# Performance work log

Measured on AMD Instinct MI355X. Metric: run time of the kernel, lower is better.

The kernel has to match this reference:

```python
import jax, jax.numpy as jnp
import numpy as np

B, TQ, TK = 4, 256, 256
Q, K, H = 256, 256, 256


def setup_inputs() -> dict:
    key = jax.random.key(0)
    ks = jax.random.split(key, 10)
    s = 0.05
    return {
        "queries": jax.random.normal(ks[0], (B, TQ, Q), dtype=jnp.float32),
        "keys": jax.random.normal(ks[1], (B, TK, K), dtype=jnp.float32),
        # lengths in [T//2, T] so no fully-masked query rows (torch would NaN there too)
        "query_lengths": jax.random.randint(ks[2], (B,), TQ // 2, TQ + 1),
        "key_lengths": jax.random.randint(ks[3], (B,), TK // 2, TK + 1),
        # nn.Linear(Q+K, H): weight applied as x @ W1; torch concat order is [keys, queries]
        "W1": jax.random.normal(ks[4], (K + Q, H), dtype=jnp.float32) * s,
        "b1": jax.random.normal(ks[5], (H,), dtype=jnp.float32) * s,
        "W2": jax.random.normal(ks[6], (H, H), dtype=jnp.float32) * s,
        "b2": jax.random.normal(ks[7], (H,), dtype=jnp.float32) * s,
        "W3": jax.random.normal(ks[8], (H, 1), dtype=jnp.float32) * s,
        "b3": jax.random.normal(ks[9], (1,), dtype=jnp.float32) * s,
    }


def reference(queries, keys, query_lengths, key_lengths, W1, b1, W2, b2, W3, b3):
    Bn, Tq, Qd = queries.shape
    Tk, Kd = keys.shape[1], keys.shape[2]
    # Split the first linear: concat([keys, queries]) @ W1 == keys@W1[:K] + queries@W1[K:]
    kh = jnp.einsum("bkd,dh->bkh", keys, W1[:Kd])      # [B,Tk,H]
    qh = jnp.einsum("bqd,dh->bqh", queries, W1[Kd:])   # [B,Tq,H]
    h = jax.nn.relu(qh[:, :, None, :] + kh[:, None, :, :] + b1)  # [B,Tq,Tk,H]
    h = jax.nn.relu(jnp.einsum("bqkh,hg->bqkg", h, W2) + b2)     # [B,Tq,Tk,H]
    scores = jnp.einsum("bqkh,h->bqk", h, W3[:, 0]) + b3[0]       # [B,Tq,Tk]
    # mask True where position is padding (query OR key out of range)
    mask = (jnp.arange(Tq)[None, :, None] >= query_lengths[:, None, None]) | (
        jnp.arange(Tk)[None, None, :] >= key_lengths[:, None, None]
    )
    scores = jnp.where(mask, -1e30, scores)
    probs = jax.nn.softmax(scores, axis=-1)
    probs = jnp.where(mask, 0.0, probs)
    return jnp.einsum("bqk,bkd->bqd", probs, keys)  # [B,Tq,K]
```

## Files before the change

### kernel.cpp

```cpp
#include <hip/hip_runtime.h>
#include <cstdint>

#define BATCH 4
#define TQ 256
#define TK 256
#define DIM 256
#define HD 256

typedef _Float16 f16x8 __attribute__((ext_vector_type(8)));
typedef float f32x4 __attribute__((ext_vector_type(4)));

union U4H8 { uint4 u; f16x8 v; };

#define KEEP(x) asm volatile("" : "+v"(x))

__device__ __forceinline__ unsigned short f2h(float f) {
    _Float16 h = (_Float16)f;
    unsigned short u;
    __builtin_memcpy(&u, &h, 2);
    return u;
}

__device__ __forceinline__ uint32_t pk2h(float a, float b) {
    auto r = __builtin_amdgcn_cvt_pkrtz(a, b);
    uint32_t w;
    __builtin_memcpy(&w, &r, 4);
    return w;
}

__global__ __launch_bounds__(256) void prep_all(
    const float* __restrict__ queries, const float* __restrict__ keys,
    const float* __restrict__ W1, const float* __restrict__ b1,
    const float* __restrict__ W2,
    float* __restrict__ qh, float* __restrict__ kh,
    unsigned short* __restrict__ W2T) {
    int i = blockIdx.x;
    int t = threadIdx.x;
    if (i >= 512) {
        __shared__ float tile[32][33];
        int bi = i - 512;
        int tx = t & 31, ty = t >> 5;
        int tc = (bi & 7) * 32, tn = (bi >> 3) * 32;
#pragma unroll
        for (int r = 0; r < 4; ++r)
            tile[ty + r * 8][tx] = W2[(tc + ty + r * 8) * HD + tn + tx];
        __syncthreads();
#pragma unroll
        for (int r = 0; r < 4; ++r)
            W2T[(tn + ty + r * 8) * HD + tc + tx] = f2h(tile[tx][ty + r * 8]);
        return;
    }
    bool isQ = i < 256;
    int r0 = (i & 255) * 4;
    const float* X = isQ ? queries : keys;
    const float* W = W1 + (isQ ? DIM * HD : 0);
    float* O = isQ ? qh : kh;
    __shared__ float xs[4][DIM];
#pragma unroll
    for (int r = 0; r < 4; ++r) xs[r][t] = X[(r0 + r) * DIM + t];
    __syncthreads();
    float acc[4] = {0.f, 0.f, 0.f, 0.f};
#pragma unroll 8
    for (int d = 0; d < DIM; ++d) {
        float w = W[d * HD + t];
#pragma unroll
        for (int r = 0; r < 4; ++r) acc[r] = fmaf(xs[r][d], w, acc[r]);
    }
    float bias = isQ ? b1[t] : 0.f;
#pragma unroll
    for (int r = 0; r < 4; ++r) O[(r0 + r) * HD + t] = acc[r] + bias;
}

__global__ __launch_bounds__(256, 2) void mlp_attn(
    const float* __restrict__ qh, const float* __restrict__ kh,
    const unsigned short* __restrict__ W2T,
    const float* __restrict__ b2, const float* __restrict__ W3,
    const float* __restrict__ keys,
    const int* __restrict__ qlens, const int* __restrict__ klens,
    float* __restrict__ out) {
    int orig = blockIdx.x;
    int bid = ((orig & 7) << 6) | (orig >> 3);
    int b = bid >> 7;
    int q0 = (bid & 127) << 1;
    int t = threadIdx.x;
    int qlen = qlens[b];
    float* orow = out + (b * TQ + q0) * DIM;
    if (q0 >= qlen) { orow[t] = 0.f; orow[DIM + t] = 0.f; return; }
    bool v1 = (q0 + 1) < qlen;
    int klen = klens[b];
    int nch = (klen + 31) >> 5;

    __shared__ uint4 Afrag[2][8][4][64];
    __shared__ float sprt[4][2][TK];
    __shared__ float srow[2][TK];
    __shared__ float Qlds[2][HD];
    __shared__ float red[16];

    int w = t >> 6, lane = t & 63;
    int col = lane & 15, quad = lane >> 4;

    int nb = w << 6;
    uint4 bfr[4][8];
#pragma unroll
    for (int nt = 0; nt < 4; ++nt) {
        int n = nb + (nt << 4) + col;
        const uint4* r = (const uint4*)(W2T + n * HD) + quad;
#pragma unroll
        for (int s = 0; s < 8; ++s) bfr[nt][s] = r[s * 4];
    }
    float b2v[4][4], w3v[4][4];
#pragma unroll
    for (int nt = 0; nt < 4; ++nt)
#pragma unroll
        for (int r = 0; r < 4; ++r) {
            int n = nb + (nt << 4) + (quad << 2) + r;
            b2v[nt][r] = b2[n];
            w3v[nt][r] = W3[n];
        }

    int qsel = w >> 1;
    int rsub = ((w & 1) << 4) | col;
    const float* kbase = kh + (b * TK + rsub) * HD + (quad << 3);

    {
        const float* qrowg = qh + (b * TQ + q0 + qsel) * HD + (quad << 3);
        const float* krow = kbase;
        uint4* as = &Afrag[0][0][w][lane];
#pragma unroll
        for (int s = 0; s < 8; ++s) {
            const float4 k0 = *(const float4*)(krow + s * 32);
            const float4 k1 = *(const float4*)(krow + s * 32 + 4);
            const float4 qa = *(const float4*)(qrowg + s * 32);
            const float4 qb = *(const float4*)(qrowg + s * 32 + 4);
            uint4 wv;
            wv.x = pk2h(fmaxf(k0.x + qa.x, 0.f), fmaxf(k0.y + qa.y, 0.f));
            wv.y = pk2h(fmaxf(k0.z + qa.z, 0.f), fmaxf(k0.w + qa.w, 0.f));
            wv.z = pk2h(fmaxf(k1.x + qb.x, 0.f), fmaxf(k1.y + qb.y, 0.f));
            wv.w = pk2h(fmaxf(k1.z + qb.z, 0.f), fmaxf(k1.w + qb.w, 0.f));
            as[s * 256] = wv;
        }
    }
    Qlds[0][t] = qh[(b * TQ + q0) * HD + t];
    Qlds[1][t] = qh[(b * TQ + q0 + 1) * HD + t];

#pragma unroll
    for (int nt = 0; nt < 4; ++nt)
#pragma unroll
        for (int s = 0; s < 8; ++s) {
            KEEP(bfr[nt][s].x); KEEP(bfr[nt][s].y);
            KEEP(bfr[nt][s].z); KEEP(bfr[nt][s].w);
        }

    __syncthreads();

    auto sloop = [&](int cur, int mt, f32x4* acc) {
#pragma unroll
        for (int s = 0; s < 8; ++s) {
            U4H8 au;
            au.u = Afrag[cur][s][mt][lane];
#pragma unroll
            for (int nt = 0; nt < 4; ++nt) {
                U4H8 bu;
                bu.u = bfr[nt][s];
                acc[nt] = __builtin_amdgcn_mfma_f32_16x16x32_f16(
                    bu.v, au.v, acc[nt], 0, 0, 0);
            }
        }
    };
    auto epi = [&](int c, int mt, const f32x4* acc) {
        int hf = mt >> 1, m2 = mt & 1;
        float part = 0.f;
#pragma unroll
        for (int nt = 0; nt < 4; ++nt)
#pragma unroll
            for (int r = 0; r < 4; ++r)
                part = fmaf(fmaxf(acc[nt][r] + b2v[nt][r], 0.f), w3v[nt][r], part);
        part += __shfl_xor(part, 16, 64);
        part += __shfl_xor(part, 32, 64);
        if (quad == 0)
            sprt[w][hf][(c << 5) | (m2 << 4) | col] = part;
    };

    for (int c = 0; c < nch; ++c) {
        int cur = c & 1;
        bool stg = (c + 1 < nch);
        const float* krow = kbase + (((c + 1) << 5)) * HD;
        uint4* as1 = &Afrag[cur ^ 1][0][w][lane];

        auto wslot = [&](int s, const float4& k0, const float4& k1) {
            const float4 qa = *(const float4*)&Qlds[qsel][s * 32 + (quad << 3)];
            const float4 qb = *(const float4*)&Qlds[qsel][s * 32 + (quad << 3) + 4];
            uint4 wv;
            wv.x = pk2h(fmaxf(k0.x + qa.x, 0.f), fmaxf(k0.y + qa.y, 0.f));
            wv.y = pk2h(fmaxf(k0.z + qa.z, 0.f), fmaxf(k0.w + qa.w, 0.f));
            wv.z = pk2h(fmaxf(k1.x + qb.x, 0.f), fmaxf(k1.y + qb.y, 0.f));
            wv.w = pk2h(fmaxf(k1.z + qb.z, 0.f), fmaxf(k1.w + qb.w, 0.f));
            as1[s * 256] = wv;
        };

        float4 A0, A1, A2, A3, B0, B1, B2, B3;
        if (stg) {
            A0 = *(const float4*)(krow);       A1 = *(const float4*)(krow + 4);
            A2 = *(const float4*)(krow + 32);  A3 = *(const float4*)(krow + 36);
        }
        __builtin_amdgcn_sched_barrier(0);

        {
            f32x4 acc[4] = {};
            sloop(cur, 0, acc);
            if (stg) {
                wslot(0, A0, A1); wslot(1, A2, A3);
                B0 = *(const float4*)(krow + 64);  B1 = *(const float4*)(krow + 68);
                B2 = *(const float4*)(krow + 96);  B3 = *(const float4*)(krow + 100);
            }
            __builtin_amdgcn_sched_barrier(0);
            epi(c, 0, acc);
            if (stg) {
                wslot(2, B0, B1); wslot(3, B2, B3);
                A0 = *(const float4*)(krow + 128); A1 = *(const float4*)(krow + 132);
                A2 = *(const float4*)(krow + 160); A3 = *(const float4*)(krow + 164);
            }
            __builtin_amdgcn_sched_barrier(0);
        }
        {
            f32x4 acc[4] = {};
            sloop(cur, 1, acc);
            if (stg) {
                wslot(4, A0, A1); wslot(5, A2, A3);
                B0 = *(const float4*)(krow + 192); B1 = *(const float4*)(krow + 196);
                B2 = *(const float4*)(krow + 224); B3 = *(const float4*)(krow + 228);
            }
            __builtin_amdgcn_sched_barrier(0);
            epi(c, 1, acc);
            if (stg) { wslot(6, B0, B1); wslot(7, B2, B3); }
        }
        {
            f32x4 acc[4] = {};
            sloop(cur, 2, acc);
            epi(c, 2, acc);
        }
        {
            f32x4 acc[4] = {};
            sloop(cur, 3, acc);
            epi(c, 3, acc);
        }
        __syncthreads();
    }

    float s0 = -3.4e38f, s1 = -3.4e38f;
    if (t < klen) {
        s0 = (sprt[0][0][t] + sprt[1][0][t]) + (sprt[2][0][t] + sprt[3][0][t]);
        s1 = (sprt[0][1][t] + sprt[1][1][t]) + (sprt[2][1][t] + sprt[3][1][t]);
    }
    float m0 = s0, m1 = s1;
#pragma unroll
    for (int off = 1; off < 64; off <<= 1) {
        m0 = fmaxf(m0, __shfl_xor(m0, off, 64));
        m1 = fmaxf(m1, __shfl_xor(m1, off, 64));
    }
    if (lane == 0) { red[w] = m0; red[8 + w] = m1; }
    __syncthreads();
    m0 = fmaxf(fmaxf(red[0], red[1]), fmaxf(red[2], red[3]));
    m1 = fmaxf(fmaxf(red[8], red[9]), fmaxf(red[10], red[11]));
    float e0 = (t < klen) ? __expf(s0 - m0) : 0.f;
    float e1 = (t < klen) ? __expf(s1 - m1) : 0.f;
    float u0 = e0, u1 = e1;
#pragma unroll
    for (int off = 1; off < 64; off <<= 1) {
        u0 += __shfl_xor(u0, off, 64);
        u1 += __shfl_xor(u1, off, 64);
    }
    if (lane == 0) { red[4 + w] = u0; red[12 + w] = u1; }
    __syncthreads();
    float d0 = red[4] + red[5] + red[6] + red[7];
    float d1 = red[12] + red[13] + red[14] + red[15];
    srow[0][t] = e0 / d0;
    srow[1][t] = e1 / d1;
    __syncthreads();

    float a0 = 0.f, a1 = 0.f;
    const float* kp = keys + b * TK * DIM + t;
#pragma unroll 8
    for (int k = 0; k < klen; ++k) {
        float v = kp[k * DIM];
        a0 = fmaf(srow[0][k], v, a0);
        a1 = fmaf(srow[1][k], v, a1);
    }
    orow[t] = a0;
    orow[DIM + t] = v1 ? a1 : 0.f;
}

extern "C" void kernel_launch(void* const* d_in, const int* in_sizes, int n_in,
                              void* d_out, int out_size, void* d_ws, size_t ws_size,
                              hipStream_t stream) {
    (void)in_sizes; (void)n_in; (void)out_size; (void)ws_size;
    const float* queries = (const float*)d_in[0];
    const float* keys    = (const float*)d_in[1];
    const int*   qlens   = (const int*)d_in[2];
    const int*   klens   = (const int*)d_in[3];
    const float* W1      = (const float*)d_in[4];
    const float* b1      = (const float*)d_in[5];
    const float* W2      = (const float*)d_in[6];
    const float* b2      = (const float*)d_in[7];
    const float* W3      = (const float*)d_in[8];
    float* out = (float*)d_out;

    float* qh = (float*)d_ws;
    float* kh = qh + BATCH * TQ * HD;
    unsigned short* W2T = (unsigned short*)(kh + BATCH * TK * HD);

    prep_all<<<576, 256, 0, stream>>>(queries, keys, W1, b1, W2, qh, kh, W2T);
    mlp_attn<<<BATCH * TQ / 2, 256, 0, stream>>>(
        qh, kh, W2T, b2, W3, keys, qlens, klens, out);
}
```

Baseline: 129.8 us.

## Use atomic work-queue persistent blocks with smaller 16-key chunks

The attention kernel now pulls (batch, query-pair) tasks from a global atomic counter that prep_all resets, instead of a fixed block-to-task mapping. Inactive query pairs finish quickly and free the block for other work. The key chunk size drops from 32 to 16 rows, and each wave builds half the A-fragment slices. This is meant to balance load across batches whose valid lengths differ and to cut the shared memory per block. The cost is two extra barriers plus an atomic per task, and twice as many chunk iterations, each with its own barrier.

```diff
diff --git a/kernel.cpp b/kernel.cpp
--- a/kernel.cpp
+++ b/kernel.cpp
@@ -6,6 +6,7 @@
 #define TK 256
 #define DIM 256
 #define HD 256
+#define NTASK 512
 
 typedef _Float16 f16x8 __attribute__((ext_vector_type(8)));
 typedef float f32x4 __attribute__((ext_vector_type(4)));
@@ -33,10 +34,11 @@
     const float* __restrict__ W1, const float* __restrict__ b1,
     const float* __restrict__ W2,
     float* __restrict__ qh, float* __restrict__ kh,
-    unsigned short* __restrict__ W2T) {
+    unsigned short* __restrict__ W2T, int* __restrict__ cnt) {
     int i = blockIdx.x;
     int t = threadIdx.x;
     if (i >= 512) {
+        if (i == 512 && t == 0) *cnt = 0;
         __shared__ float tile[32][33];
         int bi = i - 512;
         int tx = t & 31, ty = t >> 5;
@@ -77,38 +79,28 @@
     const float* __restrict__ b2, const float* __restrict__ W3,
     const float* __restrict__ keys,
     const int* __restrict__ qlens, const int* __restrict__ klens,
-    float* __restrict__ out) {
-    int orig = blockIdx.x;
-    int bid = ((orig & 7) << 6) | (orig >> 3);
-    int b = bid >> 7;
-    int q0 = (bid & 127) << 1;
+    float* __restrict__ out, int* __restrict__ gcnt) {
     int t = threadIdx.x;
-    int qlen = qlens[b];
-    float* orow = out + (b * TQ + q0) * DIM;
-    if (q0 >= qlen) { orow[t] = 0.f; orow[DIM + t] = 0.f; return; }
-    bool v1 = (q0 + 1) < qlen;
-    int klen = klens[b];
-    int nch = (klen + 31) >> 5;
-
-    __shared__ uint4 Afrag[2][8][4][64];
+    int w = t >> 6, lane = t & 63;
+    int col = lane & 15, quad = lane >> 4;
+
+    __shared__ uint4 Afrag[2][8][2][64];
     __shared__ float sprt[4][2][TK];
     __shared__ float srow[2][TK];
     __shared__ float Qlds[2][HD];
     __shared__ float red[16];
-
-    int w = t >> 6, lane = t & 63;
-    int col = lane & 15, quad = lane >> 4;
+    __shared__ int tsk;
 
     int nb = w << 6;
-    uint4 bfr[4][8];
+    uint4 afr[4][8];
+    float b2v[4][4], w3v[4][4];
 #pragma unroll
     for (int nt = 0; nt < 4; ++nt) {
         int n = nb + (nt << 4) + col;
         const uint4* r = (const uint4*)(W2T + n * HD) + quad;
 #pragma unroll
-        for (int s = 0; s < 8; ++s) bfr[nt][s] = r[s * 4];
+        for (int s = 0; s < 8; ++s) afr[nt][s] = r[s * 4];
     }
-    float b2v[4][4], w3v[4][4];
 #pragma unroll
     for (int nt = 0; nt < 4; ++nt)
 #pragma unroll
@@ -117,58 +109,32 @@
             b2v[nt][r] = b2[n];
             w3v[nt][r] = W3[n];
         }
-
-    int qsel = w >> 1;
-    int rsub = ((w & 1) << 4) | col;
-    const float* kbase = kh + (b * TK + rsub) * HD + (quad << 3);
-
-    {
-        const float* qrowg = qh + (b * TQ + q0 + qsel) * HD + (quad << 3);
-        const float* krow = kbase;
-        uint4* as = &Afrag[0][0][w][lane];
+#pragma unroll
+    for (int nt = 0; nt < 4; ++nt)
 #pragma unroll
         for (int s = 0; s < 8; ++s) {
-            const float4 k0 = *(const float4*)(krow + s * 32);
-            const float4 k1 = *(const float4*)(krow + s * 32 + 4);
-            const float4 qa = *(const float4*)(qrowg + s * 32);
-            const float4 qb = *(const float4*)(qrowg + s * 32 + 4);
-            uint4 wv;
-            wv.x = pk2h(fmaxf(k0.x + qa.x, 0.f), fmaxf(k0.y + qa.y, 0.f));
-            wv.y = pk2h(fmaxf(k0.z + qa.z, 0.f), fmaxf(k0.w + qa.w, 0.f));
-            wv.z = pk2h(fmaxf(k1.x + qb.x, 0.f), fmaxf(k1.y + qb.y, 0.f));
-            wv.w = pk2h(fmaxf(k1.z + qb.z, 0.f), fmaxf(k1.w + qb.w, 0.f));
-            as[s * 256] = wv;
-        }
-    }
-    Qlds[0][t] = qh[(b * TQ + q0) * HD + t];
-    Qlds[1][t] = qh[(b * TQ + q0 + 1) * HD + t];
-
-#pragma unroll
-    for (int nt = 0; nt < 4; ++nt)
-#pragma unroll
-        for (int s = 0; s < 8; ++s) {
-            KEEP(bfr[nt][s].x); KEEP(bfr[nt][s].y);
-            KEEP(bfr[nt][s].z); KEEP(bfr[nt][s].w);
-        }
-
-    __syncthreads();
-
-    auto sloop = [&](int cur, int mt, f32x4* acc) {
+            KEEP(afr[nt][s].x); KEEP(afr[nt][s].y);
+            KEEP(afr[nt][s].z); KEEP(afr[nt][s].w);
+        }
+
+    int mt = w >> 1;
+    int sb = (w & 1) << 2;
+
+    auto sloop = [&](int cur, int p, f32x4* acc) {
 #pragma unroll
         for (int s = 0; s < 8; ++s) {
             U4H8 au;
-            au.u = Afrag[cur][s][mt][lane];
+            au.u = Afrag[cur][s][p][lane];
 #pragma unroll
             for (int nt = 0; nt < 4; ++nt) {
                 U4H8 bu;
-                bu.u = bfr[nt][s];
+                bu.u = afr[nt][s];
                 acc[nt] = __builtin_amdgcn_mfma_f32_16x16x32_f16(
                     bu.v, au.v, acc[nt], 0, 0, 0);
             }
         }
     };
-    auto epi = [&](int c, int mt, const f32x4* acc) {
-        int hf = mt >> 1, m2 = mt & 1;
+    auto epi = [&](int c, int p, const f32x4* acc) {
         float part = 0.f;
 #pragma unroll
         for (int nt = 0; nt < 4; ++nt)
@@ -178,116 +144,139 @@
         part += __shfl_xor(part, 16, 64);
         part += __shfl_xor(part, 32, 64);
         if (quad == 0)
-            sprt[w][hf][(c << 5) | (m2 << 4) | col] = part;
+            sprt[w][p][(c << 4) | col] = part;
     };
 
-    for (int c = 0; c < nch; ++c) {
-        int cur = c & 1;
-        bool stg = (c + 1 < nch);
-        const float* krow = kbase + (((c + 1) << 5)) * HD;
-        uint4* as1 = &Afrag[cur ^ 1][0][w][lane];
-
-        auto wslot = [&](int s, const float4& k0, const float4& k1) {
-            const float4 qa = *(const float4*)&Qlds[qsel][s * 32 + (quad << 3)];
-            const float4 qb = *(const float4*)&Qlds[qsel][s * 32 + (quad << 3) + 4];
-            uint4 wv;
-            wv.x = pk2h(fmaxf(k0.x + qa.x, 0.f), fmaxf(k0.y + qa.y, 0.f));
-            wv.y = pk2h(fmaxf(k0.z + qa.z, 0.f), fmaxf(k0.w + qa.w, 0.f));
-            wv.z = pk2h(fmaxf(k1.x + qb.x, 0.f), fmaxf(k1.y + qb.y, 0.f));
-            wv.w = pk2h(fmaxf(k1.z + qb.z, 0.f), fmaxf(k1.w + qb.w, 0.f));
-            as1[s * 256] = wv;
-        };
-
-        float4 A0, A1, A2, A3, B0, B1, B2, B3;
-        if (stg) {
-            A0 = *(const float4*)(krow);       A1 = *(const float4*)(krow + 4);
-            A2 = *(const float4*)(krow + 32);  A3 = *(const float4*)(krow + 36);
-        }
-        __builtin_amdgcn_sched_barrier(0);
+    for (;;) {
+        if (t == 0) tsk = atomicAdd(gcnt, 1);
+        __syncthreads();
+        int task = tsk;
+        __syncthreads();
+        if (task >= NTASK) break;
+        int b = task >> 7;
+        int q0 = (task & 127) << 1;
+        int qlen = qlens[b];
+        float* orow = out + ((size_t)b * TQ + q0) * DIM;
+        if (q0 >= qlen) { orow[t] = 0.f; orow[DIM + t] = 0.f; continue; }
+        bool v1 = (q0 + 1) < qlen;
+        int klen = klens[b];
+        int nch = (klen + 15) >> 4;
+
+        const float* kb_t = kh + ((size_t)b * TK + col) * HD + (quad << 3);
 
         {
-            f32x4 acc[4] = {};
-            sloop(cur, 0, acc);
+            const float* qg = qh + ((size_t)b * TQ + q0 + mt) * HD + (quad << 3);
+            uint4* as = &Afrag[0][0][mt][lane];
+#pragma unroll
+            for (int j = 0; j < 4; ++j) {
+                int s = sb + j;
+                const float4 k0 = *(const float4*)(kb_t + s * 32);
+                const float4 k1 = *(const float4*)(kb_t + s * 32 + 4);
+                const float4 qa = *(const float4*)(qg + s * 32);
+                const float4 qb = *(const float4*)(qg + s * 32 + 4);
+                uint4 wv;
+                wv.x = pk2h(fmaxf(k0.x + qa.x, 0.f), fmaxf(k0.y + qa.y, 0.f));
+                wv.y = pk2h(fmaxf(k0.z + qa.z, 0.f), fmaxf(k0.w + qa.w, 0.f));
+                wv.z = pk2h(fmaxf(k1.x + qb.x, 0.f), fmaxf(k1.y + qb.y, 0.f));
+                wv.w = pk2h(fmaxf(k1.z + qb.z, 0.f), fmaxf(k1.w + qb.w, 0.f));
+                as[s * 128] = wv;
+            }
+        }
+        Qlds[0][t] = qh[((size_t)b * TQ + q0) * HD + t];
+        Qlds[1][t] = qh[((size_t)b * TQ + q0 + 1) * HD + t];
+        __syncthreads();
+
+        for (int c = 0; c < nch; ++c) {
+            int cur = c & 1;
+            bool stg = (c + 1 < nch);
+            const float* kr = kb_t + (((c + 1) << 4)) * HD;
+            uint4* as1 = &Afrag[cur ^ 1][0][mt][lane];
+
+            auto wslot = [&](int s, const float4& k0, const float4& k1) {
+                const float4 qa = *(const float4*)&Qlds[mt][s * 32 + (quad << 3)];
+                const float4 qb = *(const float4*)&Qlds[mt][s * 32 + (quad << 3) + 4];
+                uint4 wv;
+                wv.x = pk2h(fmaxf(k0.x + qa.x, 0.f), fmaxf(k0.y + qa.y, 0.f));
+                wv.y = pk2h(fmaxf(k0.z + qa.z, 0.f), fmaxf(k0.w + qa.w, 0.f));
+                wv.z = pk2h(fmaxf(k1.x + qb.x, 0.f), fmaxf(k1.y + qb.y, 0.f));
+                wv.w = pk2h(fmaxf(k1.z + qb.z, 0.f), fmaxf(k1.w + qb.w, 0.f));
+                as1[s * 128] = wv;
+            };
+
+            float4 A0, A1, A2, A3, B0, B1, B2, B3;
             if (stg) {
-                wslot(0, A0, A1); wslot(1, A2, A3);
-                B0 = *(const float4*)(krow + 64);  B1 = *(const float4*)(krow + 68);
-                B2 = *(const float4*)(krow + 96);  B3 = *(const float4*)(krow + 100);
+                A0 = *(const float4*)(kr + sb * 32);
+                A1 = *(const float4*)(kr + sb * 32 + 4);
+                A2 = *(const float4*)(kr + (sb + 1) * 32);
+                A3 = *(const float4*)(kr + (sb + 1) * 32 + 4);
             }
             __builtin_amdgcn_sched_barrier(0);
-            epi(c, 0, acc);
-            if (stg) {
-                wslot(2, B0, B1); wslot(3, B2, B3);
-                A0 = *(const float4*)(krow + 128); A1 = *(const float4*)(krow + 132);
-                A2 = *(const float4*)(krow + 160); A3 = *(const float4*)(krow + 164);
-            }
-            __builtin_amdgcn_sched_barrier(0);
-        }
-        {
-            f32x4 acc[4] = {};
-            sloop(cur, 1, acc);
-            if (stg) {
-                wslot(4, A0, A1); wslot(5, A2, A3);
-                B0 = *(const float4*)(krow + 192); B1 = *(const float4*)(krow + 196);
-                B2 = *(const float4*)(krow + 224); B3 = *(const float4*)(krow + 228);
-            }
-            __builtin_amdgcn_sched_barrier(0);
-            epi(c, 1, acc);
-            if (stg) { wslot(6, B0, B1); wslot(7, B2, B3); }
-        }
-        {
-            f32x4 acc[4] = {};
-            sloop(cur, 2, acc);
-            epi(c, 2, acc);
-        }
-        {
-            f32x4 acc[4] = {};
-            sloop(cur, 3, acc);
-            epi(c, 3, acc);
-        }
-        __syncthreads();
+
+            {
+                f32x4 acc[4] = {};
+                sloop(cur, 0, acc);
+                if (stg) {
+                    wslot(sb, A0, A1); wslot(sb + 1, A2, A3);
+                    B0 = *(const float4*)(kr + (sb + 2) * 32);
+                    B1 = *(const float4*)(kr + (sb + 2) * 32 + 4);
+                    B2 = *(const float4*)(kr + (sb + 3) * 32);
+                    B3 = *(const float4*)(kr + (sb + 3) * 32 + 4);
+                }
+                __builtin_amdgcn_sched_barrier(0);
+                epi(c, 0, acc);
+            }
+            {
+                f32x4 acc[4] = {};
+                sloop(cur, 1, acc);
+                if (stg) { wslot(sb + 2, B0, B1); wslot(sb + 3, B2, B3); }
+                __builtin_amdgcn_sched_barrier(0);
+                epi(c, 1, acc);
+            }
+            __syncthreads();
+        }
+
+        float s0 = -3.4e38f, s1 = -3.4e38f;
+        if (t < klen) {
+            s0 = (sprt[0][0][t] + sprt[1][0][t]) + (sprt[2][0][t] + sprt[3][0][t]);
+            s1 = (sprt[0][1][t] + sprt[1][1][t]) + (sprt[2][1][t] + sprt[3][1][t]);
+        }
+        float m0 = s0, m1 = s1;
+#pragma unroll
+        for (int off = 1; off < 64; off <<= 1) {
+            m0 = fmaxf(m0, __shfl_xor(m0, off, 64));
+            m1 = fmaxf(m1, __shfl_xor(m1, off, 64));
+        }
+        if (lane == 0) { red[w] = m0; red[8 + w] = m1; }
+        __syncthreads();
+        m0 = fmaxf(fmaxf(red[0], red[1]), fmaxf(red[2], red[3]));
+        m1 = fmaxf(fmaxf(red[8], red[9]), fmaxf(red[10], red[11]));
+        float e0 = (t < klen) ? __expf(s0 - m0) : 0.f;
+        float e1 = (t < klen) ? __expf(s1 - m1) : 0.f;
+        float u0 = e0, u1 = e1;
+#pragma unroll
+        for (int off = 1; off < 64; off <<= 1) {
+            u0 += __shfl_xor(u0, off, 64);
+            u1 += __shfl_xor(u1, off, 64);
+        }
+        if (lane == 0) { red[4 + w] = u0; red[12 + w] = u1; }
+        __syncthreads();
+        float d0 = red[4] + red[5] + red[6] + red[7];
+        float d1 = red[12] + red[13] + red[14] + red[15];
+        srow[0][t] = e0 / d0;
+        srow[1][t] = e1 / d1;
+        __syncthreads();
+
+        float a0 = 0.f, a1 = 0.f;
+        const float* kp = keys + (size_t)b * TK * DIM + t;
+#pragma unroll 8
+        for (int k = 0; k < klen; ++k) {
+            float v = kp[k * DIM];
+            a0 = fmaf(srow[0][k], v, a0);
+            a1 = fmaf(srow[1][k], v, a1);
+        }
+        orow[t] = a0;
+        orow[DIM + t] = v1 ? a1 : 0.f;
     }
-
-    float s0 = -3.4e38f, s1 = -3.4e38f;
-    if (t < klen) {
-        s0 = (sprt[0][0][t] + sprt[1][0][t]) + (sprt[2][0][t] + sprt[3][0][t]);
-        s1 = (sprt[0][1][t] + sprt[1][1][t]) + (sprt[2][1][t] + sprt[3][1][t]);
-    }
-    float m0 = s0, m1 = s1;
-#pragma unroll
-    for (int off = 1; off < 64; off <<= 1) {
-        m0 = fmaxf(m0, __shfl_xor(m0, off, 64));
-        m1 = fmaxf(m1, __shfl_xor(m1, off, 64));
-    }
-    if (lane == 0) { red[w] = m0; red[8 + w] = m1; }
-    __syncthreads();
-    m0 = fmaxf(fmaxf(red[0], red[1]), fmaxf(red[2], red[3]));
-    m1 = fmaxf(fmaxf(red[8], red[9]), fmaxf(red[10], red[11]));
-    float e0 = (t < klen) ? __expf(s0 - m0) : 0.f;
-    float e1 = (t < klen) ? __expf(s1 - m1) : 0.f;
-    float u0 = e0, u1 = e1;
-#pragma unroll
-    for (int off = 1; off < 64; off <<= 1) {
-        u0 += __shfl_xor(u0, off, 64);
-        u1 += __shfl_xor(u1, off, 64);
-    }
-    if (lane == 0) { red[4 + w] = u0; red[12 + w] = u1; }
-    __syncthreads();
-    float d0 = red[4] + red[5] + red[6] + red[7];
-    float d1 = red[12] + red[13] + red[14] + red[15];
-    srow[0][t] = e0 / d0;
-    srow[1][t] = e1 / d1;
-    __syncthreads();
-
-    float a0 = 0.f, a1 = 0.f;
-    const float* kp = keys + b * TK * DIM + t;
-#pragma unroll 8
-    for (int k = 0; k < klen; ++k) {
-        float v = kp[k * DIM];
-        a0 = fmaf(srow[0][k], v, a0);
-        a1 = fmaf(srow[1][k], v, a1);
-    }
-    orow[t] = a0;
-    orow[DIM + t] = v1 ? a1 : 0.f;
 }
 
 extern "C" void kernel_launch(void* const* d_in, const int* in_sizes, int n_in,
@@ -308,8 +297,9 @@
     float* qh = (float*)d_ws;
     float* kh = qh + BATCH * TQ * HD;
     unsigned short* W2T = (unsigned short*)(kh + BATCH * TK * HD);
-
-    prep_all<<<576, 256, 0, stream>>>(queries, keys, W1, b1, W2, qh, kh, W2T);
-    mlp_attn<<<BATCH * TQ / 2, 256, 0, stream>>>(
-        qh, kh, W2T, b2, W3, keys, qlens, klens, out);
-}
+    int* cnt = (int*)(W2T + HD * HD);
+
+    prep_all<<<576, 256, 0, stream>>>(queries, keys, W1, b1, W2, qh, kh, W2T, cnt);
+    mlp_attn<<<512, 256, 0, stream>>>(
+        qh, kh, W2T, b2, W3, keys, qlens, klens, out, cnt);
+}
```

Result: slower. 165.4 us (+27.4%).
